# Kernel optimization log

Hardware: AMD Instinct MI355X
Metric: run time of the kernel (lower is better)

## Reference

```python
import jax, jax.numpy as jnp
import numpy as np

N_NODES = 100000
N_FEAT = 256
OUT_DIM = 128
NNZ_X = 1_600_000
NNZ_A = 1_600_000
DROPOUT = 0.0  # layer default; floor(1-p+u) mask is all-ones -> deterministic


def setup_inputs() -> dict:
    key = jax.random.key(0)
    k = jax.random.split(key, 7)
    feat_rows = jax.random.randint(k[0], (NNZ_X,), 0, N_NODES, dtype=jnp.int32)
    feat_cols = jax.random.randint(k[1], (NNZ_X,), 0, N_FEAT, dtype=jnp.int32)
    feat_vals = jax.random.normal(k[2], (NNZ_X,), dtype=jnp.float32)
    adj_rows = jax.random.randint(k[3], (NNZ_A,), 0, N_NODES, dtype=jnp.int32)
    adj_cols = jax.random.randint(k[4], (NNZ_A,), 0, N_NODES, dtype=jnp.int32)
    adj_vals = jax.random.uniform(k[5], (NNZ_A,), dtype=jnp.float32)
    glorot_std = np.sqrt(2.0 / (N_FEAT + OUT_DIM)).astype(np.float32)
    W = jax.random.normal(k[6], (N_FEAT, OUT_DIM), dtype=jnp.float32) * glorot_std
    return {
        "feat_rows": feat_rows, "feat_cols": feat_cols, "feat_vals": feat_vals,
        "adj_rows": adj_rows, "adj_cols": adj_cols, "adj_vals": adj_vals,
        "W": W, "n_nodes": N_NODES,
    }


def reference(feat_rows, feat_cols, feat_vals, adj_rows, adj_cols, adj_vals, W, n_nodes):
    # sparse dropout on feature nonzeros: mask = floor((1-p) + uniform) in {0,1}
    u = jax.random.uniform(jax.random.key(1), feat_vals.shape, dtype=feat_vals.dtype)
    keep = jnp.floor((1.0 - DROPOUT) + u)
    vals = feat_vals * keep * (1.0 / (1.0 - DROPOUT))
    # X @ W : gather W rows by feature column, scale by nnz value, scatter-add into node rows
    xw = jax.ops.segment_sum(vals[:, None] * W[feat_cols], feat_rows,
                             num_segments=n_nodes)  # [N, D]
    # A @ (X @ W) : gather node rows by edge source, scale by edge weight, scatter-add to dest
    agg = jax.ops.segment_sum(adj_vals[:, None] * xw[adj_cols], adj_rows,
                              num_segments=n_nodes)  # [N, D]
    return jax.nn.relu(agg)
```

## Files before the change

kernel.cpp:

```cpp
#include <hip/hip_runtime.h>
#include <hip/hip_fp16.h>

#define OUT_DIM 128
#define NPS 256
#define NS_MAX 400
#define CAP_S 4608
#define SBLK1 256
#define EPT1 16
#define CHUNK1 (SBLK1 * EPT1)
#define SBLK2 256
#define GBLK 256

__global__ __launch_bounds__(SBLK1) void scatter1_kernel(
    const int* __restrict__ adj_rows, const int* __restrict__ adj_cols,
    const float* __restrict__ adj_vals, int nnz_a, int nCkA,
    const int* __restrict__ feat_rows, const int* __restrict__ feat_cols,
    const float* __restrict__ feat_vals, int nnz_x,
    int* __restrict__ cur, int2* __restrict__ pay, int ns)
{
    __shared__ int2 s_stage[CHUNK1];
    __shared__ unsigned short s_bin[CHUNK1];
    __shared__ int s_hist[NS_MAX];
    __shared__ int s_excl[NS_MAX];
    __shared__ int s_gbase[NS_MAX];

    int tid = threadIdx.x;
    bool isA = ((int)blockIdx.x < nCkA);
    const int* rows; const int* cols; const float* vals;
    int nnz, start, matbase;
    if (isA) {
        rows = adj_rows; cols = adj_cols; vals = adj_vals; nnz = nnz_a;
        start = (int)blockIdx.x * CHUNK1; matbase = 0;
    } else {
        rows = feat_rows; cols = feat_cols; vals = feat_vals; nnz = nnz_x;
        start = ((int)blockIdx.x - nCkA) * CHUNK1; matbase = ns;
    }
    int total = nnz - start; if (total > CHUNK1) total = CHUNK1;

    for (int i = tid; i < ns; i += SBLK1) s_hist[i] = 0;
    __syncthreads();

    int rr[EPT1]; int cc[EPT1]; float vv[EPT1];
    #pragma unroll
    for (int k = 0; k < EPT1; ++k) {
        int e = start + k * SBLK1 + tid;
        rr[k] = -1;
        if (e < nnz) {
            rr[k] = rows[e]; cc[k] = cols[e]; vv[k] = vals[e];
            atomicAdd(&s_hist[rr[k] >> 8], 1);
        }
    }
    __syncthreads();

    if (tid < 64) {
        int carry = 0;
        for (int seg = 0; seg < ns; seg += 64) {
            int idx = seg + tid;
            int x = (idx < ns) ? s_hist[idx] : 0;
            int incl = x;
            #pragma unroll
            for (int off = 1; off < 64; off <<= 1) {
                int y = __shfl_up(incl, off, 64);
                if (tid >= off) incl += y;
            }
            if (idx < ns) s_excl[idx] = carry + incl - x;
            carry += __shfl(incl, 63, 64);
        }
    }
    __syncthreads();

    for (int i = tid; i < ns; i += SBLK1) {
        int c = s_hist[i];
        s_gbase[i] = (c > 0) ? atomicAdd(&cur[matbase + i], c) : 0;
        s_hist[i] = 0;
    }
    __syncthreads();

    #pragma unroll
    for (int k = 0; k < EPT1; ++k) {
        if (rr[k] >= 0) {
            int b = rr[k] >> 8;
            int rl = rr[k] & 255;
            int pos = s_excl[b] + atomicAdd(&s_hist[b], 1);
            s_stage[pos] = make_int2((rl << 17) | cc[k], __float_as_int(vv[k]));
            s_bin[pos] = (unsigned short)b;
        }
    }
    __syncthreads();

    for (int i = tid; i < total; i += SBLK1) {
        int b = s_bin[i];
        int g = s_gbase[b] + (i - s_excl[b]);
        if (g < CAP_S)
            pay[(size_t)(matbase + b) * CAP_S + g] = s_stage[i];
    }
}

__global__ __launch_bounds__(SBLK2) void sort2_kernel(
    const int* __restrict__ cur, int2* __restrict__ pay,
    int2* __restrict__ row_span, int ns, int n_nodes)
{
    __shared__ int2 sedge[CAP_S];
    __shared__ int s_cnt[NPS];
    int b = blockIdx.x;
    int tid = threadIdx.x;
    int count = cur[b]; if (count > CAP_S) count = CAP_S;
    int2* region = pay + (size_t)b * CAP_S;

    s_cnt[tid] = 0;
    __syncthreads();
    for (int i = tid; i < count; i += SBLK2) {
        int2 e = region[i];
        sedge[i] = e;
        atomicAdd(&s_cnt[((unsigned)e.x) >> 17], 1);
    }
    __syncthreads();
    int v = s_cnt[tid];
    for (int off = 1; off < NPS; off <<= 1) {
        int t = (tid >= off) ? s_cnt[tid - off] : 0;
        __syncthreads();
        s_cnt[tid] += t;
        __syncthreads();
    }
    int excl = s_cnt[tid] - v;
    int m = (b >= ns) ? 1 : 0;
    int g = (b - m * ns) * NPS + tid;
    if (g < n_nodes)
        row_span[(size_t)m * n_nodes + g] = make_int2(b * CAP_S + excl, v);
    __syncthreads();
    s_cnt[tid] = excl;
    __syncthreads();
    for (int i = tid; i < count; i += SBLK2) {
        int2 e = sedge[i];
        int rl = ((unsigned)e.x) >> 17;
        int pos = atomicAdd(&s_cnt[rl], 1);
        region[pos] = make_int2(e.x & 0x1FFFF, e.y);
    }
}

__global__ void wcast_kernel(const float* __restrict__ W, __half* __restrict__ W16, int n) {
    int i = blockIdx.x * blockDim.x + threadIdx.x;
    if (i < n) W16[i] = __float2half(W[i]);
}

__global__ __launch_bounds__(GBLK) void gather_xw_kernel(
    const int2* __restrict__ row_span, const int2* __restrict__ pay,
    const __half* __restrict__ W16, __half* __restrict__ XW, int n_nodes)
{
    int tid = threadIdx.x;
    int lane = tid & 15;
    int node = blockIdx.x * 16 + (tid >> 4);
    if (node >= n_nodes) return;
    int2 span = row_span[(size_t)n_nodes + node];
    int s = span.x, cnt = span.y;
    const int4* Wv = (const int4*)W16;
    float a0=0,a1=0,a2=0,a3=0,a4=0,a5=0,a6=0,a7=0;
    for (int base = 0; base < cnt; base += 16) {
        int2 pl = make_int2(0, 0);
        if (base + lane < cnt) pl = pay[s + base + lane];
        int4 w[16];
        #pragma unroll
        for (int j = 0; j < 16; ++j) {
            int c = __shfl(pl.x, j, 16);
            w[j] = Wv[(size_t)((c << 4) | lane)];
        }
        #pragma unroll
        for (int j = 0; j < 16; ++j) {
            float v = __int_as_float(__shfl(pl.y, j, 16));
            union { int4 i4; __half2 h[4]; } u;
            u.i4 = w[j];
            float2 f0 = __half22float2(u.h[0]);
            float2 f1 = __half22float2(u.h[1]);
            float2 f2 = __half22float2(u.h[2]);
            float2 f3 = __half22float2(u.h[3]);
            a0 += v * f0.x; a1 += v * f0.y; a2 += v * f1.x; a3 += v * f1.y;
            a4 += v * f2.x; a5 += v * f2.y; a6 += v * f3.x; a7 += v * f3.y;
        }
    }
    union { int4 i4; __half2 h[4]; } o;
    o.h[0] = __floats2half2_rn(a0, a1);
    o.h[1] = __floats2half2_rn(a2, a3);
    o.h[2] = __floats2half2_rn(a4, a5);
    o.h[3] = __floats2half2_rn(a6, a7);
    ((int4*)(XW + (size_t)node * OUT_DIM))[lane] = o.i4;
}

__global__ __launch_bounds__(GBLK) void gather_agg_kernel(
    const int2* __restrict__ row_span, const int2* __restrict__ pay,
    const __half* __restrict__ XW, float* __restrict__ out, int n_nodes)
{
    int tid = threadIdx.x;
    int lane = tid & 15;
    int node = blockIdx.x * 16 + (tid >> 4);
    if (node >= n_nodes) return;
    int2 span = row_span[node];
    int s = span.x, cnt = span.y;
    const int4* Xv = (const int4*)XW;
    float a0=0,a1=0,a2=0,a3=0,a4=0,a5=0,a6=0,a7=0;
    for (int base = 0; base < cnt; base += 16) {
        int2 pl = make_int2(0, 0);
        if (base + lane < cnt) pl = pay[s + base + lane];
        int4 w[16];
        #pragma unroll
        for (int j = 0; j < 16; ++j) {
            int c = __shfl(pl.x, j, 16);
            w[j] = Xv[(size_t)((c << 4) | lane)];
        }
        #pragma unroll
        for (int j = 0; j < 16; ++j) {
            float v = __int_as_float(__shfl(pl.y, j, 16));
            union { int4 i4; __half2 h[4]; } u;
            u.i4 = w[j];
            float2 f0 = __half22float2(u.h[0]);
            float2 f1 = __half22float2(u.h[1]);
            float2 f2 = __half22float2(u.h[2]);
            float2 f3 = __half22float2(u.h[3]);
            a0 += v * f0.x; a1 += v * f0.y; a2 += v * f1.x; a3 += v * f1.y;
            a4 += v * f2.x; a5 += v * f2.y; a6 += v * f3.x; a7 += v * f3.y;
        }
    }
    float4 lo, hi;
    lo.x = fmaxf(a0, 0.f); lo.y = fmaxf(a1, 0.f);
    lo.z = fmaxf(a2, 0.f); lo.w = fmaxf(a3, 0.f);
    hi.x = fmaxf(a4, 0.f); hi.y = fmaxf(a5, 0.f);
    hi.z = fmaxf(a6, 0.f); hi.w = fmaxf(a7, 0.f);
    float4* orow = (float4*)(out + (size_t)node * OUT_DIM);
    orow[2 * lane]     = lo;
    orow[2 * lane + 1] = hi;
}

extern "C" void kernel_launch(void* const* d_in, const int* in_sizes, int n_in,
                              void* d_out, int out_size, void* d_ws, size_t ws_size,
                              hipStream_t stream) {
    const int*   feat_rows = (const int*)d_in[0];
    const int*   feat_cols = (const int*)d_in[1];
    const float* feat_vals = (const float*)d_in[2];
    const int*   adj_rows  = (const int*)d_in[3];
    const int*   adj_cols  = (const int*)d_in[4];
    const float* adj_vals  = (const float*)d_in[5];
    const float* W         = (const float*)d_in[6];
    float*       out       = (float*)d_out;

    const int nnz_x   = in_sizes[0];
    const int nnz_a   = in_sizes[3];
    const int n_w     = in_sizes[6];
    const int n_nodes = out_size / OUT_DIM;
    const int ns      = (n_nodes + NPS - 1) / NPS;

    char* p = (char*)d_ws;
    __half* XW   = (__half*)p;  p += (size_t)n_nodes * OUT_DIM * sizeof(__half);
    __half* W16  = (__half*)p;  p += (size_t)n_w * sizeof(__half);
    p = (char*)(((uintptr_t)p + 15) & ~(uintptr_t)15);
    int2* pay    = (int2*)p;    p += (size_t)2 * ns * CAP_S * sizeof(int2);
    int2* row_span = (int2*)p;  p += (size_t)2 * n_nodes * sizeof(int2);
    int* cur     = (int*)p;     p += (size_t)2 * ns * sizeof(int);

    hipMemsetAsync(cur, 0, (size_t)2 * ns * sizeof(int), stream);

    wcast_kernel<<<(n_w + 255) / 256, 256, 0, stream>>>(W, W16, n_w);

    const int nCkA = (nnz_a + CHUNK1 - 1) / CHUNK1;
    const int nCkX = (nnz_x + CHUNK1 - 1) / CHUNK1;
    scatter1_kernel<<<nCkA + nCkX, SBLK1, 0, stream>>>(
        adj_rows, adj_cols, adj_vals, nnz_a, nCkA,
        feat_rows, feat_cols, feat_vals, nnz_x,
        cur, pay, ns);

    sort2_kernel<<<2 * ns, SBLK2, 0, stream>>>(cur, pay, row_span, ns, n_nodes);

    const int gnb = (n_nodes + 15) / 16;
    gather_xw_kernel<<<gnb, GBLK, 0, stream>>>(row_span, pay, W16, XW, n_nodes);
    gather_agg_kernel<<<gnb, GBLK, 0, stream>>>(row_span, pay, XW, out, n_nodes);
}
```

Measured before the change: 249.8 us.

## Register-stage sort buckets, warp-scan offsets, read fp32 W directly, prefetch agg payload

The bucket sort kernel now holds each thread's edges in registers instead of a large shared staging array. Its block-wide Hillis-Steele scan is replaced by a single-wave shuffle scan. The fp16 cast kernel for W is removed, and the XW gather reads fp32 W rows directly with a variable-length inner loop, which drops one launch. The aggregation gather prefetches the next 16-entry payload chunk while it consumes the current one and adds an occupancy hint. The trade-offs are higher register pressure, and twice the bytes read per W gather (W is small and likely cache-resident).

```diff
diff --git a/kernel.cpp b/kernel.cpp
--- a/kernel.cpp
+++ b/kernel.cpp
@@ -5,6 +5,7 @@
 #define NPS 256
 #define NS_MAX 400
 #define CAP_S 4608
+#define EPT2 18
 #define SBLK1 256
 #define EPT1 16
 #define CHUNK1 (SBLK1 * EPT1)
@@ -100,8 +101,8 @@
     const int* __restrict__ cur, int2* __restrict__ pay,
     int2* __restrict__ row_span, int ns, int n_nodes)
 {
-    __shared__ int2 sedge[CAP_S];
     __shared__ int s_cnt[NPS];
+    __shared__ int s_excl[NPS];
     int b = blockIdx.x;
     int tid = threadIdx.x;
     int count = cur[b]; if (count > CAP_S) count = CAP_S;
@@ -109,43 +110,55 @@
 
     s_cnt[tid] = 0;
     __syncthreads();
-    for (int i = tid; i < count; i += SBLK2) {
-        int2 e = region[i];
-        sedge[i] = e;
-        atomicAdd(&s_cnt[((unsigned)e.x) >> 17], 1);
-    }
-    __syncthreads();
-    int v = s_cnt[tid];
-    for (int off = 1; off < NPS; off <<= 1) {
-        int t = (tid >= off) ? s_cnt[tid - off] : 0;
-        __syncthreads();
-        s_cnt[tid] += t;
-        __syncthreads();
-    }
-    int excl = s_cnt[tid] - v;
+
+    int2 er[EPT2];
+    #pragma unroll
+    for (int k = 0; k < EPT2; ++k) {
+        int i = tid + k * SBLK2;
+        er[k] = make_int2(-1, 0);
+        if (i < count) {
+            er[k] = region[i];
+            atomicAdd(&s_cnt[((unsigned)er[k].x) >> 17], 1);
+        }
+    }
+    __syncthreads();
+
+    if (tid < 64) {
+        int carry = 0;
+        #pragma unroll
+        for (int seg = 0; seg < NPS; seg += 64) {
+            int x = s_cnt[seg + tid];
+            int incl = x;
+            #pragma unroll
+            for (int off = 1; off < 64; off <<= 1) {
+                int y = __shfl_up(incl, off, 64);
+                if (tid >= off) incl += y;
+            }
+            s_excl[seg + tid] = carry + incl - x;
+            carry += __shfl(incl, 63, 64);
+        }
+    }
+    __syncthreads();
+
     int m = (b >= ns) ? 1 : 0;
     int g = (b - m * ns) * NPS + tid;
     if (g < n_nodes)
-        row_span[(size_t)m * n_nodes + g] = make_int2(b * CAP_S + excl, v);
-    __syncthreads();
-    s_cnt[tid] = excl;
-    __syncthreads();
-    for (int i = tid; i < count; i += SBLK2) {
-        int2 e = sedge[i];
-        int rl = ((unsigned)e.x) >> 17;
-        int pos = atomicAdd(&s_cnt[rl], 1);
-        region[pos] = make_int2(e.x & 0x1FFFF, e.y);
-    }
-}
-
-__global__ void wcast_kernel(const float* __restrict__ W, __half* __restrict__ W16, int n) {
-    int i = blockIdx.x * blockDim.x + threadIdx.x;
-    if (i < n) W16[i] = __float2half(W[i]);
+        row_span[(size_t)m * n_nodes + g] = make_int2(b * CAP_S + s_excl[tid], s_cnt[tid]);
+    __syncthreads();
+
+    #pragma unroll
+    for (int k = 0; k < EPT2; ++k) {
+        if (er[k].x >= 0) {
+            int rl = ((unsigned)er[k].x) >> 17;
+            int pos = atomicAdd(&s_excl[rl], 1);
+            region[pos] = make_int2(er[k].x & 0x1FFFF, er[k].y);
+        }
+    }
 }
 
 __global__ __launch_bounds__(GBLK) void gather_xw_kernel(
     const int2* __restrict__ row_span, const int2* __restrict__ pay,
-    const __half* __restrict__ W16, __half* __restrict__ XW, int n_nodes)
+    const float* __restrict__ W, __half* __restrict__ XW, int n_nodes)
 {
     int tid = threadIdx.x;
     int lane = tid & 15;
@@ -153,17 +166,53 @@
     if (node >= n_nodes) return;
     int2 span = row_span[(size_t)n_nodes + node];
     int s = span.x, cnt = span.y;
-    const int4* Wv = (const int4*)W16;
+    const float4* Wv = (const float4*)W;
     float a0=0,a1=0,a2=0,a3=0,a4=0,a5=0,a6=0,a7=0;
     for (int base = 0; base < cnt; base += 16) {
+        int mm = cnt - base; if (mm > 16) mm = 16;
         int2 pl = make_int2(0, 0);
-        if (base + lane < cnt) pl = pay[s + base + lane];
+        if (lane < mm) pl = pay[s + base + lane];
+        #pragma unroll 4
+        for (int j = 0; j < mm; ++j) {
+            int c = __shfl(pl.x, j, 16);
+            float v = __int_as_float(__shfl(pl.y, j, 16));
+            float4 f0 = Wv[c * 32 + lane * 2];
+            float4 f1 = Wv[c * 32 + lane * 2 + 1];
+            a0 += v * f0.x; a1 += v * f0.y; a2 += v * f0.z; a3 += v * f0.w;
+            a4 += v * f1.x; a5 += v * f1.y; a6 += v * f1.z; a7 += v * f1.w;
+        }
+    }
+    union { int4 i4; __half2 h[4]; } o;
+    o.h[0] = __floats2half2_rn(a0, a1);
+    o.h[1] = __floats2half2_rn(a2, a3);
+    o.h[2] = __floats2half2_rn(a4, a5);
+    o.h[3] = __floats2half2_rn(a6, a7);
+    ((int4*)(XW + (size_t)node * OUT_DIM))[lane] = o.i4;
+}
+
+__global__ __launch_bounds__(GBLK, 4) void gather_agg_kernel(
+    const int2* __restrict__ row_span, const int2* __restrict__ pay,
+    const __half* __restrict__ XW, float* __restrict__ out, int n_nodes)
+{
+    int tid = threadIdx.x;
+    int lane = tid & 15;
+    int node = blockIdx.x * 16 + (tid >> 4);
+    if (node >= n_nodes) return;
+    int2 span = row_span[node];
+    int s = span.x, cnt = span.y;
+    const int4* Xv = (const int4*)XW;
+    float a0=0,a1=0,a2=0,a3=0,a4=0,a5=0,a6=0,a7=0;
+    int2 pl = make_int2(0, 0);
+    if (lane < cnt) pl = pay[s + lane];
+    for (int base = 0; base < cnt; base += 16) {
         int4 w[16];
         #pragma unroll
         for (int j = 0; j < 16; ++j) {
             int c = __shfl(pl.x, j, 16);
-            w[j] = Wv[(size_t)((c << 4) | lane)];
-        }
+            w[j] = Xv[(size_t)((c << 4) | lane)];
+        }
+        int2 pln = make_int2(0, 0);
+        if (base + 16 + lane < cnt) pln = pay[s + base + 16 + lane];
         #pragma unroll
         for (int j = 0; j < 16; ++j) {
             float v = __int_as_float(__shfl(pl.y, j, 16));
@@ -176,48 +225,7 @@
             a0 += v * f0.x; a1 += v * f0.y; a2 += v * f1.x; a3 += v * f1.y;
             a4 += v * f2.x; a5 += v * f2.y; a6 += v * f3.x; a7 += v * f3.y;
         }
-    }
-    union { int4 i4; __half2 h[4]; } o;
-    o.h[0] = __floats2half2_rn(a0, a1);
-    o.h[1] = __floats2half2_rn(a2, a3);
-    o.h[2] = __floats2half2_rn(a4, a5);
-    o.h[3] = __floats2half2_rn(a6, a7);
-    ((int4*)(XW + (size_t)node * OUT_DIM))[lane] = o.i4;
-}
-
-__global__ __launch_bounds__(GBLK) void gather_agg_kernel(
-    const int2* __restrict__ row_span, const int2* __restrict__ pay,
-    const __half* __restrict__ XW, float* __restrict__ out, int n_nodes)
-{
-    int tid = threadIdx.x;
-    int lane = tid & 15;
-    int node = blockIdx.x * 16 + (tid >> 4);
-    if (node >= n_nodes) return;
-    int2 span = row_span[node];
-    int s = span.x, cnt = span.y;
-    const int4* Xv = (const int4*)XW;
-    float a0=0,a1=0,a2=0,a3=0,a4=0,a5=0,a6=0,a7=0;
-    for (int base = 0; base < cnt; base += 16) {
-        int2 pl = make_int2(0, 0);
-        if (base + lane < cnt) pl = pay[s + base + lane];
-        int4 w[16];
-        #pragma unroll
-        for (int j = 0; j < 16; ++j) {
-            int c = __shfl(pl.x, j, 16);
-            w[j] = Xv[(size_t)((c << 4) | lane)];
-        }
-        #pragma unroll
-        for (int j = 0; j < 16; ++j) {
-            float v = __int_as_float(__shfl(pl.y, j, 16));
-            union { int4 i4; __half2 h[4]; } u;
-            u.i4 = w[j];
-            float2 f0 = __half22float2(u.h[0]);
-            float2 f1 = __half22float2(u.h[1]);
-            float2 f2 = __half22float2(u.h[2]);
-            float2 f3 = __half22float2(u.h[3]);
-            a0 += v * f0.x; a1 += v * f0.y; a2 += v * f1.x; a3 += v * f1.y;
-            a4 += v * f2.x; a5 += v * f2.y; a6 += v * f3.x; a7 += v * f3.y;
-        }
+        pl = pln;
     }
     float4 lo, hi;
     lo.x = fmaxf(a0, 0.f); lo.y = fmaxf(a1, 0.f);
@@ -243,21 +251,17 @@
 
     const int nnz_x   = in_sizes[0];
     const int nnz_a   = in_sizes[3];
-    const int n_w     = in_sizes[6];
     const int n_nodes = out_size / OUT_DIM;
     const int ns      = (n_nodes + NPS - 1) / NPS;
 
     char* p = (char*)d_ws;
     __half* XW   = (__half*)p;  p += (size_t)n_nodes * OUT_DIM * sizeof(__half);
-    __half* W16  = (__half*)p;  p += (size_t)n_w * sizeof(__half);
     p = (char*)(((uintptr_t)p + 15) & ~(uintptr_t)15);
     int2* pay    = (int2*)p;    p += (size_t)2 * ns * CAP_S * sizeof(int2);
     int2* row_span = (int2*)p;  p += (size_t)2 * n_nodes * sizeof(int2);
     int* cur     = (int*)p;     p += (size_t)2 * ns * sizeof(int);
 
     hipMemsetAsync(cur, 0, (size_t)2 * ns * sizeof(int), stream);
-
-    wcast_kernel<<<(n_w + 255) / 256, 256, 0, stream>>>(W, W16, n_w);
 
     const int nCkA = (nnz_a + CHUNK1 - 1) / CHUNK1;
     const int nCkX = (nnz_x + CHUNK1 - 1) / CHUNK1;
@@ -269,6 +273,6 @@
     sort2_kernel<<<2 * ns, SBLK2, 0, stream>>>(cur, pay, row_span, ns, n_nodes);
 
     const int gnb = (n_nodes + 15) / 16;
-    gather_xw_kernel<<<gnb, GBLK, 0, stream>>>(row_span, pay, W16, XW, n_nodes);
+    gather_xw_kernel<<<gnb, GBLK, 0, stream>>>(row_span, pay, W, XW, n_nodes);
     gather_agg_kernel<<<gnb, GBLK, 0, stream>>>(row_span, pay, XW, out, n_nodes);
 }
```

New measurement: 252.9 us. No clear change (+1.2%).

## Fuse per-bucket row sort into gather kernels using shared-memory staging

Applied to the files above, without the earlier changes.

Removes the separate sort2 pass and the row_span array. Each gather kernel now loads its bucket's edges, counting-sorts them by local row in LDS for one half of the bucket (128 nodes), and gathers directly from shared memory. This eliminates a global read-write round trip of the payload and one launch. In exchange, each bucket is read twice (once per half block), there are only about 800 blocks, and a fixed LDS cap (CAPH) could drop edges if a half-bucket overflows.

```diff
diff --git a/kernel.cpp b/kernel.cpp
--- a/kernel.cpp
+++ b/kernel.cpp
@@ -5,10 +5,12 @@
 #define NPS 256
 #define NS_MAX 400
 #define CAP_S 4608
+#define HNPS 128
+#define CAPH 2560
+#define EPTF 18
 #define SBLK1 256
 #define EPT1 16
 #define CHUNK1 (SBLK1 * EPT1)
-#define SBLK2 256
 #define GBLK 256
 
 __global__ __launch_bounds__(SBLK1) void scatter1_kernel(
@@ -96,137 +98,211 @@
     }
 }
 
-__global__ __launch_bounds__(SBLK2) void sort2_kernel(
-    const int* __restrict__ cur, int2* __restrict__ pay,
-    int2* __restrict__ row_span, int ns, int n_nodes)
-{
-    __shared__ int2 sedge[CAP_S];
-    __shared__ int s_cnt[NPS];
-    int b = blockIdx.x;
-    int tid = threadIdx.x;
-    int count = cur[b]; if (count > CAP_S) count = CAP_S;
-    int2* region = pay + (size_t)b * CAP_S;
-
-    s_cnt[tid] = 0;
-    __syncthreads();
-    for (int i = tid; i < count; i += SBLK2) {
-        int2 e = region[i];
-        sedge[i] = e;
-        atomicAdd(&s_cnt[((unsigned)e.x) >> 17], 1);
-    }
-    __syncthreads();
-    int v = s_cnt[tid];
-    for (int off = 1; off < NPS; off <<= 1) {
-        int t = (tid >= off) ? s_cnt[tid - off] : 0;
-        __syncthreads();
-        s_cnt[tid] += t;
-        __syncthreads();
-    }
-    int excl = s_cnt[tid] - v;
-    int m = (b >= ns) ? 1 : 0;
-    int g = (b - m * ns) * NPS + tid;
-    if (g < n_nodes)
-        row_span[(size_t)m * n_nodes + g] = make_int2(b * CAP_S + excl, v);
-    __syncthreads();
-    s_cnt[tid] = excl;
-    __syncthreads();
-    for (int i = tid; i < count; i += SBLK2) {
-        int2 e = sedge[i];
-        int rl = ((unsigned)e.x) >> 17;
-        int pos = atomicAdd(&s_cnt[rl], 1);
-        region[pos] = make_int2(e.x & 0x1FFFF, e.y);
-    }
-}
-
 __global__ void wcast_kernel(const float* __restrict__ W, __half* __restrict__ W16, int n) {
     int i = blockIdx.x * blockDim.x + threadIdx.x;
     if (i < n) W16[i] = __float2half(W[i]);
 }
 
-__global__ __launch_bounds__(GBLK) void gather_xw_kernel(
-    const int2* __restrict__ row_span, const int2* __restrict__ pay,
-    const __half* __restrict__ W16, __half* __restrict__ XW, int n_nodes)
+__global__ __launch_bounds__(GBLK, 4) void fused_xw_kernel(
+    const int* __restrict__ cur, const int2* __restrict__ pay,
+    const __half* __restrict__ W16, __half* __restrict__ XW,
+    int ns, int n_nodes)
 {
+    __shared__ int2 s_edge[CAPH];
+    __shared__ int s_cnt[HNPS];
+    __shared__ int s_excl[HNPS];
     int tid = threadIdx.x;
+    int sb = blockIdx.x >> 1;
+    int h  = blockIdx.x & 1;
+    int count = cur[ns + sb]; if (count > CAP_S) count = CAP_S;
+    const int2* region = pay + (size_t)(ns + sb) * CAP_S;
+
+    if (tid < HNPS) s_cnt[tid] = 0;
+    __syncthreads();
+
+    int2 er[EPTF];
+    #pragma unroll
+    for (int k = 0; k < EPTF; ++k) {
+        int i = tid + k * GBLK;
+        er[k] = make_int2(-1, 0);
+        if (i < count) {
+            int2 e = region[i];
+            int rl = ((unsigned)e.x) >> 17;
+            if ((rl >> 7) == h) {
+                er[k] = e;
+                atomicAdd(&s_cnt[rl & (HNPS - 1)], 1);
+            }
+        }
+    }
+    __syncthreads();
+
+    if (tid < 64) {
+        int carry = 0;
+        #pragma unroll
+        for (int seg = 0; seg < HNPS; seg += 64) {
+            int x = s_cnt[seg + tid];
+            int incl = x;
+            #pragma unroll
+            for (int off = 1; off < 64; off <<= 1) {
+                int y = __shfl_up(incl, off, 64);
+                if (tid >= off) incl += y;
+            }
+            s_excl[seg + tid] = carry + incl - x;
+            carry += __shfl(incl, 63, 64);
+        }
+    }
+    __syncthreads();
+
+    #pragma unroll
+    for (int k = 0; k < EPTF; ++k) {
+        if (er[k].x >= 0) {
+            int rl = (((unsigned)er[k].x) >> 17) & (HNPS - 1);
+            int pos = atomicAdd(&s_excl[rl], 1);
+            if (pos < CAPH) s_edge[pos] = er[k];
+        }
+    }
+    __syncthreads();
+
     int lane = tid & 15;
-    int node = blockIdx.x * 16 + (tid >> 4);
-    if (node >= n_nodes) return;
-    int2 span = row_span[(size_t)n_nodes + node];
-    int s = span.x, cnt = span.y;
+    int grp = tid >> 4;
     const int4* Wv = (const int4*)W16;
-    float a0=0,a1=0,a2=0,a3=0,a4=0,a5=0,a6=0,a7=0;
-    for (int base = 0; base < cnt; base += 16) {
-        int2 pl = make_int2(0, 0);
-        if (base + lane < cnt) pl = pay[s + base + lane];
-        int4 w[16];
+    for (int r = grp; r < HNPS; r += 16) {
+        int node = sb * NPS + h * HNPS + r;
+        if (node >= n_nodes) break;
+        int cnt = s_cnt[r];
+        int start = s_excl[r] - cnt;
+        float a0=0,a1=0,a2=0,a3=0,a4=0,a5=0,a6=0,a7=0;
+        for (int base = 0; base < cnt; base += 16) {
+            int2 pl = make_int2(0, 0);
+            if (base + lane < cnt) pl = s_edge[start + base + lane];
+            int4 w[16];
+            #pragma unroll
+            for (int j = 0; j < 16; ++j) {
+                int c = __shfl(pl.x, j, 16) & 0x1FFFF;
+                w[j] = Wv[(c << 4) | lane];
+            }
+            #pragma unroll
+            for (int j = 0; j < 16; ++j) {
+                float v = __int_as_float(__shfl(pl.y, j, 16));
+                union { int4 i4; __half2 hh[4]; } u;
+                u.i4 = w[j];
+                float2 f0 = __half22float2(u.hh[0]);
+                float2 f1 = __half22float2(u.hh[1]);
+                float2 f2 = __half22float2(u.hh[2]);
+                float2 f3 = __half22float2(u.hh[3]);
+                a0 += v * f0.x; a1 += v * f0.y; a2 += v * f1.x; a3 += v * f1.y;
+                a4 += v * f2.x; a5 += v * f2.y; a6 += v * f3.x; a7 += v * f3.y;
+            }
+        }
+        union { int4 i4; __half2 hh[4]; } o;
+        o.hh[0] = __floats2half2_rn(a0, a1);
+        o.hh[1] = __floats2half2_rn(a2, a3);
+        o.hh[2] = __floats2half2_rn(a4, a5);
+        o.hh[3] = __floats2half2_rn(a6, a7);
+        ((int4*)(XW + (size_t)node * OUT_DIM))[lane] = o.i4;
+    }
+}
+
+__global__ __launch_bounds__(GBLK, 4) void fused_agg_kernel(
+    const int* __restrict__ cur, const int2* __restrict__ pay,
+    const __half* __restrict__ XW, float* __restrict__ out,
+    int ns, int n_nodes)
+{
+    __shared__ int2 s_edge[CAPH];
+    __shared__ int s_cnt[HNPS];
+    __shared__ int s_excl[HNPS];
+    int tid = threadIdx.x;
+    int sb = blockIdx.x >> 1;
+    int h  = blockIdx.x & 1;
+    int count = cur[sb]; if (count > CAP_S) count = CAP_S;
+    const int2* region = pay + (size_t)sb * CAP_S;
+
+    if (tid < HNPS) s_cnt[tid] = 0;
+    __syncthreads();
+
+    int2 er[EPTF];
+    #pragma unroll
+    for (int k = 0; k < EPTF; ++k) {
+        int i = tid + k * GBLK;
+        er[k] = make_int2(-1, 0);
+        if (i < count) {
+            int2 e = region[i];
+            int rl = ((unsigned)e.x) >> 17;
+            if ((rl >> 7) == h) {
+                er[k] = e;
+                atomicAdd(&s_cnt[rl & (HNPS - 1)], 1);
+            }
+        }
+    }
+    __syncthreads();
+
+    if (tid < 64) {
+        int carry = 0;
         #pragma unroll
-        for (int j = 0; j < 16; ++j) {
-            int c = __shfl(pl.x, j, 16);
-            w[j] = Wv[(size_t)((c << 4) | lane)];
-        }
-        #pragma unroll
-        for (int j = 0; j < 16; ++j) {
-            float v = __int_as_float(__shfl(pl.y, j, 16));
-            union { int4 i4; __half2 h[4]; } u;
-            u.i4 = w[j];
-            float2 f0 = __half22float2(u.h[0]);
-            float2 f1 = __half22float2(u.h[1]);
-            float2 f2 = __half22float2(u.h[2]);
-            float2 f3 = __half22float2(u.h[3]);
-            a0 += v * f0.x; a1 += v * f0.y; a2 += v * f1.x; a3 += v * f1.y;
-            a4 += v * f2.x; a5 += v * f2.y; a6 += v * f3.x; a7 += v * f3.y;
-        }
-    }
-    union { int4 i4; __half2 h[4]; } o;
-    o.h[0] = __floats2half2_rn(a0, a1);
-    o.h[1] = __floats2half2_rn(a2, a3);
-    o.h[2] = __floats2half2_rn(a4, a5);
-    o.h[3] = __floats2half2_rn(a6, a7);
-    ((int4*)(XW + (size_t)node * OUT_DIM))[lane] = o.i4;
-}
-
-__global__ __launch_bounds__(GBLK) void gather_agg_kernel(
-    const int2* __restrict__ row_span, const int2* __restrict__ pay,
-    const __half* __restrict__ XW, float* __restrict__ out, int n_nodes)
-{
-    int tid = threadIdx.x;
+        for (int seg = 0; seg < HNPS; seg += 64) {
+            int x = s_cnt[seg + tid];
+            int incl = x;
+            #pragma unroll
+            for (int off = 1; off < 64; off <<= 1) {
+                int y = __shfl_up(incl, off, 64);
+                if (tid >= off) incl += y;
+            }
+            s_excl[seg + tid] = carry + incl - x;
+            carry += __shfl(incl, 63, 64);
+        }
+    }
+    __syncthreads();
+
+    #pragma unroll
+    for (int k = 0; k < EPTF; ++k) {
+        if (er[k].x >= 0) {
+            int rl = (((unsigned)er[k].x) >> 17) & (HNPS - 1);
+            int pos = atomicAdd(&s_excl[rl], 1);
+            if (pos < CAPH) s_edge[pos] = er[k];
+        }
+    }
+    __syncthreads();
+
     int lane = tid & 15;
-    int node = blockIdx.x * 16 + (tid >> 4);
-    if (node >= n_nodes) return;
-    int2 span = row_span[node];
-    int s = span.x, cnt = span.y;
+    int grp = tid >> 4;
     const int4* Xv = (const int4*)XW;
-    float a0=0,a1=0,a2=0,a3=0,a4=0,a5=0,a6=0,a7=0;
-    for (int base = 0; base < cnt; base += 16) {
-        int2 pl = make_int2(0, 0);
-        if (base + lane < cnt) pl = pay[s + base + lane];
-        int4 w[16];
-        #pragma unroll
-        for (int j = 0; j < 16; ++j) {
-            int c = __shfl(pl.x, j, 16);
-            w[j] = Xv[(size_t)((c << 4) | lane)];
-        }
-        #pragma unroll
-        for (int j = 0; j < 16; ++j) {
-            float v = __int_as_float(__shfl(pl.y, j, 16));
-            union { int4 i4; __half2 h[4]; } u;
-            u.i4 = w[j];
-            float2 f0 = __half22float2(u.h[0]);
-            float2 f1 = __half22float2(u.h[1]);
-            float2 f2 = __half22float2(u.h[2]);
-            float2 f3 = __half22float2(u.h[3]);
-            a0 += v * f0.x; a1 += v * f0.y; a2 += v * f1.x; a3 += v * f1.y;
-            a4 += v * f2.x; a5 += v * f2.y; a6 += v * f3.x; a7 += v * f3.y;
-        }
-    }
-    float4 lo, hi;
-    lo.x = fmaxf(a0, 0.f); lo.y = fmaxf(a1, 0.f);
-    lo.z = fmaxf(a2, 0.f); lo.w = fmaxf(a3, 0.f);
-    hi.x = fmaxf(a4, 0.f); hi.y = fmaxf(a5, 0.f);
-    hi.z = fmaxf(a6, 0.f); hi.w = fmaxf(a7, 0.f);
-    float4* orow = (float4*)(out + (size_t)node * OUT_DIM);
-    orow[2 * lane]     = lo;
-    orow[2 * lane + 1] = hi;
+    for (int r = grp; r < HNPS; r += 16) {
+        int node = sb * NPS + h * HNPS + r;
+        if (node >= n_nodes) break;
+        int cnt = s_cnt[r];
+        int start = s_excl[r] - cnt;
+        float a0=0,a1=0,a2=0,a3=0,a4=0,a5=0,a6=0,a7=0;
+        for (int base = 0; base < cnt; base += 16) {
+            int2 pl = make_int2(0, 0);
+            if (base + lane < cnt) pl = s_edge[start + base + lane];
+            int4 w[16];
+            #pragma unroll
+            for (int j = 0; j < 16; ++j) {
+                int c = __shfl(pl.x, j, 16) & 0x1FFFF;
+                w[j] = Xv[(size_t)((c << 4) | lane)];
+            }
+            #pragma unroll
+            for (int j = 0; j < 16; ++j) {
+                float v = __int_as_float(__shfl(pl.y, j, 16));
+                union { int4 i4; __half2 hh[4]; } u;
+                u.i4 = w[j];
+                float2 f0 = __half22float2(u.hh[0]);
+                float2 f1 = __half22float2(u.hh[1]);
+                float2 f2 = __half22float2(u.hh[2]);
+                float2 f3 = __half22float2(u.hh[3]);
+                a0 += v * f0.x; a1 += v * f0.y; a2 += v * f1.x; a3 += v * f1.y;
+                a4 += v * f2.x; a5 += v * f2.y; a6 += v * f3.x; a7 += v * f3.y;
+            }
+        }
+        float4 lo, hi;
+        lo.x = fmaxf(a0, 0.f); lo.y = fmaxf(a1, 0.f);
+        lo.z = fmaxf(a2, 0.f); lo.w = fmaxf(a3, 0.f);
+        hi.x = fmaxf(a4, 0.f); hi.y = fmaxf(a5, 0.f);
+        hi.z = fmaxf(a6, 0.f); hi.w = fmaxf(a7, 0.f);
+        float4* orow = (float4*)(out + (size_t)node * OUT_DIM);
+        orow[2 * lane]     = lo;
+        orow[2 * lane + 1] = hi;
+    }
 }
 
 extern "C" void kernel_launch(void* const* d_in, const int* in_sizes, int n_in,
@@ -252,7 +328,6 @@
     __half* W16  = (__half*)p;  p += (size_t)n_w * sizeof(__half);
     p = (char*)(((uintptr_t)p + 15) & ~(uintptr_t)15);
     int2* pay    = (int2*)p;    p += (size_t)2 * ns * CAP_S * sizeof(int2);
-    int2* row_span = (int2*)p;  p += (size_t)2 * n_nodes * sizeof(int2);
     int* cur     = (int*)p;     p += (size_t)2 * ns * sizeof(int);
 
     hipMemsetAsync(cur, 0, (size_t)2 * ns * sizeof(int), stream);
@@ -266,9 +341,7 @@
         feat_rows, feat_cols, feat_vals, nnz_x,
         cur, pay, ns);
 
-    sort2_kernel<<<2 * ns, SBLK2, 0, stream>>>(cur, pay, row_span, ns, n_nodes);
-
-    const int gnb = (n_nodes + 15) / 16;
-    gather_xw_kernel<<<gnb, GBLK, 0, stream>>>(row_span, pay, W16, XW, n_nodes);
-    gather_agg_kernel<<<gnb, GBLK, 0, stream>>>(row_span, pay, XW, out, n_nodes);
-}
+    const int nhb = 2 * ns;
+    fused_xw_kernel<<<nhb, GBLK, 0, stream>>>(cur, pay, W16, XW, ns, n_nodes);
+    fused_agg_kernel<<<nhb, GBLK, 0, stream>>>(cur, pay, XW, out, ns, n_nodes);
+}
```

Result: slower. 256.9 us (+2.8%).
